# Performance work log

Measured on AMD Instinct MI355X. Metric: run time of the kernel, lower is better.

## Reference

```python
import jax, jax.numpy as jnp
import numpy as np

B, D = 4096, 1024
N_CLASSES = 100
INF = jnp.float32(3.4e38)


def setup_inputs() -> dict:
    key = jax.random.key(0)
    k1, k2 = jax.random.split(key)
    x = jax.random.normal(k1, (B, 1, D), dtype=jnp.float32)
    labels = jax.random.randint(k2, (B,), 0, N_CLASSES)
    return {"x": x, "labels": labels}


def _awareness_scan(xs, labels_f, R_init):
    # xs: [B, D] float32, labels_f: [B] float32
    b, d = xs.shape
    slots = jnp.arange(b)

    def step(state, inp):
        refs, ref_labels, n_refs, count, min_d, max_d, R = state
        xi, li = inp
        mask = slots < n_refs  # active reference slots
        # distances from candidate to current reference set (torch.cdist, p=2)
        d_all = jnp.sqrt(jnp.sum((refs - xi[None, :]) ** 2, axis=-1))  # [B]
        d_all = jax.lax.stop_gradient(d_all)
        d_act = jnp.where(mask, d_all, INF)
        min_act = jnp.min(d_act)
        is_first = count == 1
        # new reference iff ALL active distances exceed R (i.e. min > R)
        insert = is_first | (min_act > R)
        refs2 = jnp.where(insert, refs.at[n_refs].set(xi), refs)
        ref_labels2 = jnp.where(insert, ref_labels.at[n_refs].set(li), ref_labels)
        n_refs2 = n_refs + insert.astype(n_refs.dtype)
        # dynamic ray update (skipped on the very first sample, as in torch)
        max_act = jnp.max(jnp.where(mask, d_all, -INF))
        min_d2 = jnp.where(is_first, min_d, jnp.minimum(min_d, min_act))
        max_d2 = jnp.where(is_first, max_d, jnp.maximum(max_d, max_act))
        R2 = jnp.where(is_first, R, (min_d2 + max_d2) / 3)
        # prediction: nearest reference AFTER potential insertion
        mask2 = slots < n_refs2
        d2 = jnp.sqrt(jnp.sum((refs2 - xi[None, :]) ** 2, axis=-1))
        d2 = jax.lax.stop_gradient(d2)
        idx = jnp.argmin(jnp.where(mask2, d2, INF))
        pred = ref_labels2[idx]
        new_state = (refs2, ref_labels2, n_refs2, count + 1, min_d2, max_d2, R2)
        return new_state, pred

    init = (
        jnp.zeros((b, d), jnp.float32),   # reference instances buffer
        jnp.zeros((b,), jnp.float32),     # reference labels buffer
        jnp.int32(0),                     # n_refs
        jnp.int32(1),                     # count (starts at 1, as in torch)
        INF,                              # min_dist
        jnp.float32(0.0),                 # max_dist
        jnp.float32(R_init),              # R
    )
    _, preds = jax.lax.scan(step, init, (xs, labels_f))
    return preds  # [B] float32


def reference(x, labels):
    # x: [B, 1, D]; labels: [B] int. update_ref_insts=True, set_labels=labels.
    xs = x.reshape(x.shape[0], x.shape[2])
    labels_f = labels.astype(jnp.float32)
    return _awareness_scan(xs, labels_f, 1.0)
```

## Files before the change

kernel.cpp:

```cpp
#include <hip/hip_runtime.h>
#include <stdint.h>

#define B_N   4096
#define D_DIM 1024
#define INF_F 3.4e38f

typedef float floatx4 __attribute__((ext_vector_type(4)));

#define XQ_OFF 131072

__global__ __launch_bounds__(256)
void k_prep(const float* __restrict__ x, unsigned char* __restrict__ xq,
            float* __restrict__ norms,
            unsigned long long* __restrict__ minpack,
            unsigned int* __restrict__ maxbits) {
    const int row = blockIdx.x;
    const int t   = threadIdx.x;
    float4 v = ((const float4*)x)[row * 256 + t];
    int p = __builtin_amdgcn_cvt_pk_fp8_f32(v.x, v.y, 0, false);
    p     = __builtin_amdgcn_cvt_pk_fp8_f32(v.z, v.w, p, true);
    ((int*)xq)[row * 256 + t] = p;
    float s = v.x * v.x + v.y * v.y + v.z * v.z + v.w * v.w;
    #pragma unroll
    for (int off = 32; off; off >>= 1) s += __shfl_down(s, off);
    __shared__ float ws4[4];
    if ((t & 63) == 0) ws4[t >> 6] = s;
    __syncthreads();
    if (t == 0) {
        norms[row]   = ws4[0] + ws4[1] + ws4[2] + ws4[3];
        minpack[row] = 0xFFFFFFFFFFFFFFFFull;
        maxbits[row] = 0u;
    }
}

#define GLDS(g, l)                                                              \
    __builtin_amdgcn_global_load_lds(                                           \
        (__attribute__((address_space(1))) void*)(void*)(g),                    \
        (__attribute__((address_space(3))) void*)(void*)(l), 16, 0, 0)

__global__ __launch_bounds__(512, 6)
void k_pass1_fp8(const unsigned char* __restrict__ xq,
                 const float* __restrict__ norms,
                 unsigned long long* __restrict__ minpack,
                 unsigned int* __restrict__ maxbits) {
    int bid = blockIdx.x;
    int ti  = (int)((sqrtf(8.f * bid + 1.f) - 1.f) * 0.5f);
    while ((ti + 1) * (ti + 2) / 2 <= bid) ti++;
    while (ti * (ti + 1) / 2 > bid) ti--;
    int tj  = bid - ti * (ti + 1) / 2;

    __shared__ unsigned char As[16384];
    __shared__ unsigned char Bs[16384];
    __shared__ unsigned long long redMin[128][2];
    __shared__ float redMax[128][2];

    const int t    = threadIdx.x;
    const int w    = t >> 6, lane = t & 63;
    const int wm   = w >> 1, wn = w & 1;
    const int q4   = lane >> 4, c15 = lane & 15;
    const int i0   = ti * 128, j0 = tj * 128;

    const int sr = lane >> 3;
    const int sc = (lane & 7) ^ (sr & 7);

    const unsigned char* gA[2]; const unsigned char* gB[2];
    unsigned char* lA[2]; unsigned char* lB[2];
    #pragma unroll
    for (int q = 0; q < 2; q++) {
        int e   = w * 2 + q;
        int row = e * 8 + sr;
        gA[q] = xq + (size_t)(i0 + row) * D_DIM + sc * 16;
        gB[q] = xq + (size_t)(j0 + row) * D_DIM + sc * 16;
        lA[q] = As + e * 1024;
        lB[q] = Bs + e * 1024;
    }

    const int r7 = c15 & 7;
    int oib[4];
    #pragma unroll
    for (int kk = 0; kk < 4; kk++) {
        int sl  = kk * 2 + (q4 >> 1);
        oib[kk] = (((sl ^ r7) << 4) | ((q4 & 1) << 3));
    }
    int rbA[2], rbB[4];
    #pragma unroll
    for (int st = 0; st < 2; st++) rbA[st] = (wm * 32 + st * 16 + c15) * 128;
    #pragma unroll
    for (int st = 0; st < 4; st++) rbB[st] = (wn * 64 + st * 16 + c15) * 128;

    floatx4 acc[2][4];
    #pragma unroll
    for (int m = 0; m < 2; m++)
        #pragma unroll
        for (int n = 0; n < 4; n++)
            acc[m][n] = (floatx4){0.f, 0.f, 0.f, 0.f};

    for (int it = 0; it < 8; it++) {
        __syncthreads();
        #pragma unroll
        for (int q = 0; q < 2; q++) {
            GLDS(gA[q], lA[q]);
            GLDS(gB[q], lB[q]);
            gA[q] += 128; gB[q] += 128;
        }
        __syncthreads();
        #pragma unroll
        for (int kk = 0; kk < 4; kk++) {
            long long af[2], bfr[4];
            #pragma unroll
            for (int st = 0; st < 2; st++)
                af[st]  = *(const long long*)(As + rbA[st] + oib[kk]);
            #pragma unroll
            for (int st = 0; st < 4; st++)
                bfr[st] = *(const long long*)(Bs + rbB[st] + oib[kk]);
            #pragma unroll
            for (int m = 0; m < 2; m++)
                #pragma unroll
                for (int n = 0; n < 4; n++)
                    acc[m][n] = __builtin_amdgcn_mfma_f32_16x16x32_fp8_fp8(
                        af[m], bfr[n], acc[m][n], 0, 0, 0);
        }
    }

    float nj[4];
    #pragma unroll
    for (int st = 0; st < 4; st++) nj[st] = norms[j0 + wn * 64 + st * 16 + c15];

    #pragma unroll
    for (int st_m = 0; st_m < 2; st_m++) {
        #pragma unroll
        for (int r = 0; r < 4; r++) {
            int i_loc = wm * 32 + st_m * 16 + q4 * 4 + r;
            int gi    = i0 + i_loc;
            float ni  = norms[gi];
            unsigned long long mp = 0xFFFFFFFFFFFFFFFFull;
            float mx = -INF_F;
            #pragma unroll
            for (int st_n = 0; st_n < 4; st_n++) {
                int gj = j0 + wn * 64 + st_n * 16 + c15;
                if (gj < gi) {
                    float dot = acc[st_m][st_n][r];
                    float d2  = fmaxf(ni + nj[st_n] - 2.f * dot, 0.f);
                    unsigned long long p =
                        ((unsigned long long)__float_as_uint(d2) << 32) | (unsigned)gj;
                    if (p < mp) mp = p;
                    mx = fmaxf(mx, d2);
                }
            }
            #pragma unroll
            for (int off = 1; off < 16; off <<= 1) {
                unsigned long long op = __shfl_xor(mp, off, 64);
                if (op < mp) mp = op;
                float om = __shfl_xor(mx, off, 64);
                mx = fmaxf(mx, om);
            }
            if (c15 == 0) { redMin[i_loc][wn] = mp; redMax[i_loc][wn] = mx; }
        }
    }
    __syncthreads();
    if (t < 128) {
        unsigned long long mp = redMin[t][0];
        if (redMin[t][1] < mp) mp = redMin[t][1];
        float mx = fmaxf(redMax[t][0], redMax[t][1]);
        if (mp != 0xFFFFFFFFFFFFFFFFull) {
            atomicMin(&minpack[i0 + t], mp);
            atomicMax(&maxbits[i0 + t], __float_as_uint(mx));
        }
    }
}

__global__ __launch_bounds__(1024)
void k_tail(const unsigned long long* __restrict__ minpack,
            const unsigned int* __restrict__ maxbits,
            const float* __restrict__ x, const float* __restrict__ norms,
            const int* __restrict__ labels, int* __restrict__ ref_idx,
            float* __restrict__ out) {
    const int t    = threadIdx.x;
    const int lane = t & 63, wid = t >> 6;
    float m[4], M[4];
    #pragma unroll
    for (int q = 0; q < 4; q++) {
        int i = t * 4 + q;
        unsigned long long p = minpack[i];
        float dmin = (p == 0xFFFFFFFFFFFFFFFFull)
                       ? INF_F : sqrtf(__uint_as_float((unsigned)(p >> 32)));
        m[q] = (i == 0) ? INF_F : dmin;
        M[q] = (i == 0) ? -INF_F : sqrtf(__uint_as_float(maxbits[i]));
    }
    float pmin[4], pmax[4];
    pmin[0] = m[0]; pmax[0] = M[0];
    #pragma unroll
    for (int q = 1; q < 4; q++) {
        pmin[q] = fminf(pmin[q - 1], m[q]);
        pmax[q] = fmaxf(pmax[q - 1], M[q]);
    }
    float wmin = pmin[3], wmax = pmax[3];
    #pragma unroll
    for (int off = 1; off < 64; off <<= 1) {
        float a = __shfl_up(wmin, off, 64);
        float b = __shfl_up(wmax, off, 64);
        if (lane >= off) { wmin = fminf(wmin, a); wmax = fmaxf(wmax, b); }
    }
    __shared__ float swmin[16], swmax[16];
    if (lane == 63) { swmin[wid] = wmin; swmax[wid] = wmax; }
    __syncthreads();
    float exwMin = INF_F, exwMax = -INF_F;
    for (int k = 0; k < wid; k++) {
        exwMin = fminf(exwMin, swmin[k]);
        exwMax = fmaxf(exwMax, swmax[k]);
    }
    float upMin = __shfl_up(wmin, 1, 64);
    float upMax = __shfl_up(wmax, 1, 64);
    float exMin = fminf(exwMin, (lane > 0) ? upMin : INF_F);
    float exMax = fmaxf(exwMax, (lane > 0) ? upMax : -INF_F);

    int viol = B_N;
    #pragma unroll
    for (int q = 0; q < 4; q++) {
        int i = t * 4 + q;
        if (i >= 1) {
            float pm = (q == 0) ? exMin : fminf(exMin, pmin[q - 1]);
            float pM = (q == 0) ? exMax : fmaxf(exMax, pmax[q - 1]);
            float R  = (i == 1) ? 1.0f : (pm + pM) / 3.0f;
            if (!(m[q] > R) && i < viol) viol = i;
        }
    }
    int vw = viol;
    #pragma unroll
    for (int off = 32; off; off >>= 1) vw = min(vw, __shfl_down(vw, off, 64));
    __shared__ int svw[16];
    if (lane == 0) svw[wid] = vw;
    __syncthreads();
    int s_star = B_N;
    for (int k = 0; k < 16; k++) s_star = min(s_star, svw[k]);

    for (int i = t; i < s_star; i += 1024) out[i] = (float)labels[i];

    __shared__ float s_state[3];
    __shared__ int s_n;
    if (s_star < B_N && t == (s_star >> 2)) {
        int q = s_star & 3;
        float pm = (q == 0) ? exMin : fminf(exMin, pmin[q - 1]);
        float pM = (q == 0) ? exMax : fmaxf(exMax, pmax[q - 1]);
        float md = fminf(pm, m[q]);
        float Md = fmaxf(pM, M[q]);
        s_state[0] = md; s_state[1] = Md; s_state[2] = (md + Md) / 3.0f;
        s_n = s_star;
        unsigned long long p = minpack[s_star];
        int j = (int)(unsigned)(p & 0xFFFFFFFFu);
        out[s_star] = (float)labels[j];
    }
    if (s_star >= B_N) return;

    for (int s = t; s < s_star; s += 1024) ref_idx[s] = s;
    __syncthreads();

    __shared__ unsigned long long redp[1024];
    __shared__ float redm[1024];
    for (int i = s_star + 1; i < B_N; i++) {
        int n = s_n;
        const float* xi = x + (size_t)i * D_DIM;
        float ni = norms[i];
        unsigned long long mp = 0xFFFFFFFFFFFFFFFFull;
        float mx = -INF_F;
        for (int slot = t; slot < n; slot += 1024) {
            int j = ref_idx[slot];
            const float* xj = x + (size_t)j * D_DIM;
            float dot = 0.f;
            for (int k = 0; k < D_DIM; k++) dot = fmaf(xi[k], xj[k], dot);
            float d = sqrtf(fmaxf(ni + norms[j] - 2.f * dot, 0.f));
            unsigned long long p =
                ((unsigned long long)__float_as_uint(d) << 32) | (unsigned)slot;
            if (p < mp) mp = p;
            mx = fmaxf(mx, d);
        }
        redp[t] = mp; redm[t] = mx;
        __syncthreads();
        for (int off = 512; off; off >>= 1) {
            if (t < off) {
                if (redp[t + off] < redp[t]) redp[t] = redp[t + off];
                redm[t] = fmaxf(redm[t], redm[t + off]);
            }
            __syncthreads();
        }
        if (t == 0) {
            unsigned long long p = redp[0];
            float min_act = __uint_as_float((unsigned)(p >> 32));
            int minslot   = (int)(unsigned)(p & 0xFFFFFFFFu);
            float max_act = redm[0];
            bool insert = (min_act > s_state[2]);
            int pred;
            if (insert) {
                ref_idx[n] = i;
                s_n = n + 1;
                pred = (min_act <= 0.0f) ? labels[ref_idx[minslot]] : labels[i];
            } else {
                pred = labels[ref_idx[minslot]];
            }
            float md = fminf(s_state[0], min_act);
            float Md = fmaxf(s_state[1], max_act);
            s_state[0] = md; s_state[1] = Md; s_state[2] = (md + Md) / 3.0f;
            out[i] = (float)pred;
        }
        __syncthreads();
    }
}

extern "C" void kernel_launch(void* const* d_in, const int* in_sizes, int n_in,
                              void* d_out, int out_size, void* d_ws, size_t ws_size,
                              hipStream_t stream) {
    const float* x      = (const float*)d_in[0];
    const int*   labels = (const int*)d_in[1];
    float*       out    = (float*)d_out;
    char* ws = (char*)d_ws;
    unsigned long long* minpack = (unsigned long long*)ws;
    unsigned int*       maxbits = (unsigned int*)(ws + 32768);
    float*              norms   = (float*)(ws + 49152);
    int*                ref_idx = (int*)(ws + 65600);
    unsigned char*      xq      = (unsigned char*)(ws + XQ_OFF);

    k_prep<<<B_N, 256, 0, stream>>>(x, xq, norms, minpack, maxbits);
    const int ntiles  = B_N / 128;
    const int nblocks = ntiles * (ntiles + 1) / 2;
    k_pass1_fp8<<<nblocks, 512, 0, stream>>>(xq, norms, minpack, maxbits);
    k_tail<<<1, 1024, 0, stream>>>(minpack, maxbits, x, norms, labels, ref_idx, out);
}
```

Baseline: 98.45 us.

## Triple-buffer fp8 Gram tiles with async global-to-LDS prefetch and block swizzle

Replaces the synchronous two-barrier K loop (128-byte K chunks) with a three-stage ring of 64-byte K chunks. Loads run two stages ahead via global_load_lds, with explicit vmcnt waits and s_setprio around the MFMA section. It also remaps block IDs so consecutive blocks touch spread-out triangular tiles, and changes the LDS swizzle to match the narrower rows. The aim is to hide global load latency behind MFMA work, at the cost of more barriers per K step and hand-managed waitcnt correctness.

```diff
diff --git a/kernel.cpp b/kernel.cpp
--- a/kernel.cpp
+++ b/kernel.cpp
@@ -43,14 +43,15 @@
                  const float* __restrict__ norms,
                  unsigned long long* __restrict__ minpack,
                  unsigned int* __restrict__ maxbits) {
-    int bid = blockIdx.x;
+    int bid0 = blockIdx.x;
+    int bid  = (bid0 & 7) * 66 + (bid0 >> 3);
     int ti  = (int)((sqrtf(8.f * bid + 1.f) - 1.f) * 0.5f);
     while ((ti + 1) * (ti + 2) / 2 <= bid) ti++;
     while (ti * (ti + 1) / 2 > bid) ti--;
     int tj  = bid - ti * (ti + 1) / 2;
 
-    __shared__ unsigned char As[16384];
-    __shared__ unsigned char Bs[16384];
+    __shared__ unsigned char As[3][8192];
+    __shared__ unsigned char Bs[3][8192];
     __shared__ unsigned long long redMin[128][2];
     __shared__ float redMax[128][2];
 
@@ -60,33 +61,22 @@
     const int q4   = lane >> 4, c15 = lane & 15;
     const int i0   = ti * 128, j0 = tj * 128;
 
-    const int sr = lane >> 3;
-    const int sc = (lane & 7) ^ (sr & 7);
-
-    const unsigned char* gA[2]; const unsigned char* gB[2];
-    unsigned char* lA[2]; unsigned char* lB[2];
-    #pragma unroll
-    for (int q = 0; q < 2; q++) {
-        int e   = w * 2 + q;
-        int row = e * 8 + sr;
-        gA[q] = xq + (size_t)(i0 + row) * D_DIM + sc * 16;
-        gB[q] = xq + (size_t)(j0 + row) * D_DIM + sc * 16;
-        lA[q] = As + e * 1024;
-        lB[q] = Bs + e * 1024;
-    }
-
-    const int r7 = c15 & 7;
-    int oib[4];
-    #pragma unroll
-    for (int kk = 0; kk < 4; kk++) {
-        int sl  = kk * 2 + (q4 >> 1);
-        oib[kk] = (((sl ^ r7) << 4) | ((q4 & 1) << 3));
-    }
+    const int sr = lane >> 2;
+    const int sc = (lane & 3) ^ ((sr >> 2) & 3);
+    const unsigned char* gA = xq + (size_t)(i0 + w * 16 + sr) * D_DIM + sc * 16;
+    const unsigned char* gB = xq + (size_t)(j0 + w * 16 + sr) * D_DIM + sc * 16;
+    const int lo = w * 1024;
+
+    const int x2 = (c15 >> 2) & 3;
+    int oib[2];
+    #pragma unroll
+    for (int kk = 0; kk < 2; kk++)
+        oib[kk] = ((((kk * 2 + (q4 >> 1)) ^ x2) << 4) | ((q4 & 1) << 3));
     int rbA[2], rbB[4];
     #pragma unroll
-    for (int st = 0; st < 2; st++) rbA[st] = (wm * 32 + st * 16 + c15) * 128;
-    #pragma unroll
-    for (int st = 0; st < 4; st++) rbB[st] = (wn * 64 + st * 16 + c15) * 128;
+    for (int st = 0; st < 2; st++) rbA[st] = (wm * 32 + st * 16 + c15) * 64;
+    #pragma unroll
+    for (int st = 0; st < 4; st++) rbB[st] = (wn * 64 + st * 16 + c15) * 64;
 
     floatx4 acc[2][4];
     #pragma unroll
@@ -95,24 +85,27 @@
         for (int n = 0; n < 4; n++)
             acc[m][n] = (floatx4){0.f, 0.f, 0.f, 0.f};
 
-    for (int it = 0; it < 8; it++) {
-        __syncthreads();
+    GLDS(gA, As[0] + lo); GLDS(gB, Bs[0] + lo); gA += 64; gB += 64;
+    GLDS(gA, As[1] + lo); GLDS(gB, Bs[1] + lo); gA += 64; gB += 64;
+
+    #pragma unroll
+    for (int it = 0; it < 16; it++) {
+        if (it < 15) asm volatile("s_waitcnt vmcnt(2)" ::: "memory");
+        else         asm volatile("s_waitcnt vmcnt(0)" ::: "memory");
+        __builtin_amdgcn_s_barrier();
+
+        const unsigned char* Ap = As[it % 3];
+        const unsigned char* Bp = Bs[it % 3];
+        __builtin_amdgcn_s_setprio(1);
         #pragma unroll
-        for (int q = 0; q < 2; q++) {
-            GLDS(gA[q], lA[q]);
-            GLDS(gB[q], lB[q]);
-            gA[q] += 128; gB[q] += 128;
-        }
-        __syncthreads();
-        #pragma unroll
-        for (int kk = 0; kk < 4; kk++) {
+        for (int kk = 0; kk < 2; kk++) {
             long long af[2], bfr[4];
             #pragma unroll
             for (int st = 0; st < 2; st++)
-                af[st]  = *(const long long*)(As + rbA[st] + oib[kk]);
+                af[st]  = *(const long long*)(Ap + rbA[st] + oib[kk]);
             #pragma unroll
             for (int st = 0; st < 4; st++)
-                bfr[st] = *(const long long*)(Bs + rbB[st] + oib[kk]);
+                bfr[st] = *(const long long*)(Bp + rbB[st] + oib[kk]);
             #pragma unroll
             for (int m = 0; m < 2; m++)
                 #pragma unroll
@@ -120,6 +113,15 @@
                     acc[m][n] = __builtin_amdgcn_mfma_f32_16x16x32_fp8_fp8(
                         af[m], bfr[n], acc[m][n], 0, 0, 0);
         }
+        __builtin_amdgcn_s_setprio(0);
+
+        asm volatile("s_waitcnt lgkmcnt(0)" ::: "memory");
+        if (it < 14) {
+            GLDS(gA, As[(it + 2) % 3] + lo);
+            GLDS(gB, Bs[(it + 2) % 3] + lo);
+            gA += 64; gB += 64;
+        }
+        __builtin_amdgcn_s_barrier();
     }
 
     float nj[4];
```

New measurement: 99.52 us. No clear change (+1.1%).
